# Kernel optimization log

Hardware: AMD Instinct MI355X
Metric: run time of the kernel (lower is better)

The kernel has to match this reference:

```python
import jax, jax.numpy as jnp
import numpy as np


def setup_inputs() -> dict:
    key = jax.random.key(0)
    k1, k2, k3, k4 = jax.random.split(key, 4)
    B, N, IN_DIM, QK_DIM = 8, 2048, 10, 32
    s = jax.random.normal(k1, (B, N, IN_DIM), dtype=jnp.float32)
    G = jax.random.uniform(k2, (B, N, N), dtype=jnp.float32)
    Wq = jax.random.normal(k3, (QK_DIM, IN_DIM), dtype=jnp.float32) * (1.0 / np.sqrt(IN_DIM))
    Wk = jax.random.normal(k4, (QK_DIM, IN_DIM), dtype=jnp.float32) * (1.0 / np.sqrt(IN_DIM))
    return {"s": s, "G": G, "Wq": Wq, "Wk": Wk}


def reference(s, G, Wq, Wk):
    # q, k: [B, N, qk_dim]  (nn.Linear with no bias: x @ W^T)
    q = jnp.einsum("bnd,qd->bnq", s, Wq)
    k = jnp.einsum("bnd,qd->bnq", s, Wk)
    # logits: [B, N, N]
    logits = jnp.einsum("bnq,bmq->bnm", q, k)
    w = jnp.square(logits) * G
    w = w / (jnp.sum(w, axis=-1, keepdims=True) + 1e-06)
    return w
```

## Files before the change

kernel.cpp:

```cpp
#include <hip/hip_runtime.h>
#include <stdint.h>

#define BB 8
#define NN 2048
#define IND 10
#define QK 32

typedef float f32x4 __attribute__((ext_vector_type(4)));

__global__ __launch_bounds__(256) void qk_kernel(
    const float* __restrict__ s,
    const float* __restrict__ Wq, const float* __restrict__ Wk,
    float* __restrict__ q_ws, float* __restrict__ kt_ws) {
  int t = blockIdx.x * 256 + threadIdx.x;
  int b  = t >> 16;
  int n  = (t >> 5) & (NN - 1);
  int qd = t & 31;
  const float* srow = s + (size_t)(b * NN + n) * IND;
  float acq = 0.f, ack = 0.f;
#pragma unroll
  for (int d = 0; d < IND; ++d) {
    float sv = srow[d];
    acq = fmaf(sv, Wq[qd * IND + d], acq);
    ack = fmaf(sv, Wk[qd * IND + d], ack);
  }
  q_ws[(size_t)(b * NN + n) * QK + qd] = acq;
  int w  = n >> 9;
  int m  = n & 511;
  int i  = (m & 255) >> 2;
  int jc = ((m < 256) ? 0 : 4) + (m & 3);
  int ev = qd >> 2, c = qd & 3;
  kt_ws[(((size_t)(b * 4 + w) * 4096) + (ev * 8 + jc) * 64 + i) * 4 + c] = ack;
}

__global__ __launch_bounds__(256, 2) void attn_kernel(
    const float* __restrict__ G,
    const float* __restrict__ q_ws, const float* __restrict__ kt_ws,
    float* __restrict__ out) {
  const int tid = threadIdx.x;
  const int b = blockIdx.y;
  const int r0 = blockIdx.x * 8;
  const int w = tid >> 6, lane = tid & 63;

  __shared__ float q_lds[4][256];
  __shared__ float red[4][8];

  {
    const float* qb = q_ws + ((size_t)b * NN + r0) * QK;
    *(float4*)&q_lds[w][4 * lane] = *(const float4*)&qb[4 * lane];
  }

  float acc[8][8];
#pragma unroll
  for (int r = 0; r < 8; ++r)
#pragma unroll
    for (int j = 0; j < 8; ++j) acc[r][j] = 0.f;

  const float4* kt =
      (const float4*)kt_ws + (size_t)(b * 4 + w) * 4096 + lane;

  float4 ka[8], kb[8];
#pragma unroll
  for (int j = 0; j < 8; ++j) ka[j] = kt[j * 64];

#pragma unroll
  for (int ev = 0; ev < 8; ++ev) {
    if (ev < 7) {
#pragma unroll
      for (int j = 0; j < 8; ++j) kb[j] = kt[((ev + 1) * 8 + j) * 64];
    }
#pragma unroll
    for (int r = 0; r < 8; ++r) {
      float q4[4];
      *(float4*)q4 = *(const float4*)&q_lds[w][r * 32 + ev * 4];
#pragma unroll
      for (int j = 0; j < 8; ++j) {
        acc[r][j] = fmaf(q4[0], ka[j].x, acc[r][j]);
        acc[r][j] = fmaf(q4[1], ka[j].y, acc[r][j]);
        acc[r][j] = fmaf(q4[2], ka[j].z, acc[r][j]);
        acc[r][j] = fmaf(q4[3], ka[j].w, acc[r][j]);
      }
    }
#pragma unroll
    for (int j = 0; j < 8; ++j) ka[j] = kb[j];
  }

  const float* gb = G + ((size_t)b * NN + r0) * NN + 512 * w + 4 * lane;
  float4 g0[8], g1[8];
#pragma unroll
  for (int r = 0; r < 8; ++r) {
    g0[r] = *(const float4*)(gb + (size_t)r * NN);
    g1[r] = *(const float4*)(gb + (size_t)r * NN + 256);
  }
  __builtin_amdgcn_sched_barrier(0);

  float rsum[8];
#pragma unroll
  for (int r = 0; r < 8; ++r) {
    float gg[8];
    *(float4*)&gg[0] = g0[r];
    *(float4*)&gg[4] = g1[r];
    float sum = 0.f;
#pragma unroll
    for (int j = 0; j < 8; ++j) {
      float v = acc[r][j];
      v = v * v * gg[j];
      acc[r][j] = v;
      sum += v;
    }
#pragma unroll
    for (int off = 32; off >= 1; off >>= 1) sum += __shfl_xor(sum, off, 64);
    rsum[r] = sum;
  }

  if ((tid & 63) == 0) {
#pragma unroll
    for (int r = 0; r < 8; ++r) red[w][r] = rsum[r];
  }
  __syncthreads();

  float inv[8];
#pragma unroll
  for (int r = 0; r < 8; ++r) {
    float total = red[0][r] + red[1][r] + red[2][r] + red[3][r];
    inv[r] = 1.0f / (total + 1e-6f);
  }

  float* ob = out + ((size_t)b * NN + r0) * NN + 512 * w + 4 * lane;
#pragma unroll
  for (int r = 0; r < 8; ++r) {
    f32x4 o0, o1;
    o0.x = acc[r][0] * inv[r]; o0.y = acc[r][1] * inv[r];
    o0.z = acc[r][2] * inv[r]; o0.w = acc[r][3] * inv[r];
    o1.x = acc[r][4] * inv[r]; o1.y = acc[r][5] * inv[r];
    o1.z = acc[r][6] * inv[r]; o1.w = acc[r][7] * inv[r];
    __builtin_nontemporal_store(o0, (f32x4*)(ob + (size_t)r * NN));
    __builtin_nontemporal_store(o1, (f32x4*)(ob + (size_t)r * NN + 256));
  }
}

extern "C" void kernel_launch(void* const* d_in, const int* in_sizes, int n_in,
                              void* d_out, int out_size, void* d_ws, size_t ws_size,
                              hipStream_t stream) {
  const float* s  = (const float*)d_in[0];
  const float* G  = (const float*)d_in[1];
  const float* Wq = (const float*)d_in[2];
  const float* Wk = (const float*)d_in[3];
  float* out = (float*)d_out;

  float* q_ws  = (float*)d_ws;
  float* kt_ws = q_ws + (size_t)BB * NN * QK;

  qk_kernel<<<(BB * NN * QK) / 256, 256, 0, stream>>>(s, Wq, Wk, q_ws, kt_ws);

  dim3 grid(NN / 8, BB);
  attn_kernel<<<grid, 256, 0, stream>>>(G, q_ws, kt_ws, out);
}
```

Baseline: 62.47 us.

## Prefetch G tile via direct global-to-LDS loads overlapping final QK step

Issues the G tile loads before the last q·k accumulation step. Five rows per wave go straight into LDS via global_load_lds and three rows go into registers, so the long-latency G fetch overlaps the remaining FMAs. A vmcnt(0) wait and scheduling barriers then gate the softmax-style normalization. The intent is to hide G memory latency without blowing up register pressure, at the cost of about 40KB of extra LDS per block, which may reduce occupancy.

```diff
diff --git a/kernel.cpp b/kernel.cpp
--- a/kernel.cpp
+++ b/kernel.cpp
@@ -33,6 +33,15 @@
   kt_ws[(((size_t)(b * 4 + w) * 4096) + (ev * 8 + jc) * 64 + i) * 4 + c] = ack;
 }
 
+__device__ __forceinline__ void gload_lds16(const float* src, float* lds_dst) {
+  __builtin_amdgcn_global_load_lds(
+      reinterpret_cast<const __attribute__((address_space(1))) uint32_t*>(
+          reinterpret_cast<uintptr_t>(src)),
+      reinterpret_cast<__attribute__((address_space(3))) uint32_t*>(
+          reinterpret_cast<uintptr_t>(lds_dst)),
+      16, 0, 0);
+}
+
 __global__ __launch_bounds__(256, 2) void attn_kernel(
     const float* __restrict__ G,
     const float* __restrict__ q_ws, const float* __restrict__ kt_ws,
@@ -42,6 +51,7 @@
   const int r0 = blockIdx.x * 8;
   const int w = tid >> 6, lane = tid & 63;
 
+  __shared__ float g_lds[4][5][512];
   __shared__ float q_lds[4][256];
   __shared__ float red[4][8];
 
@@ -64,11 +74,9 @@
   for (int j = 0; j < 8; ++j) ka[j] = kt[j * 64];
 
 #pragma unroll
-  for (int ev = 0; ev < 8; ++ev) {
-    if (ev < 7) {
+  for (int ev = 0; ev < 7; ++ev) {
 #pragma unroll
-      for (int j = 0; j < 8; ++j) kb[j] = kt[((ev + 1) * 8 + j) * 64];
-    }
+    for (int j = 0; j < 8; ++j) kb[j] = kt[((ev + 1) * 8 + j) * 64];
 #pragma unroll
     for (int r = 0; r < 8; ++r) {
       float q4[4];
@@ -85,21 +93,49 @@
     for (int j = 0; j < 8; ++j) ka[j] = kb[j];
   }
 
+  __builtin_amdgcn_sched_barrier(0);
+
   const float* gb = G + ((size_t)b * NN + r0) * NN + 512 * w + 4 * lane;
-  float4 g0[8], g1[8];
+#pragma unroll
+  for (int r = 0; r < 5; ++r) {
+    gload_lds16(gb + (size_t)r * NN, &g_lds[w][r][0]);
+    gload_lds16(gb + (size_t)r * NN + 256, &g_lds[w][r][256]);
+  }
+  f32x4 g5[3][2];
+#pragma unroll
+  for (int r = 0; r < 3; ++r) {
+    g5[r][0] = *(const f32x4*)(gb + (size_t)(5 + r) * NN);
+    g5[r][1] = *(const f32x4*)(gb + (size_t)(5 + r) * NN + 256);
+  }
+  __builtin_amdgcn_sched_barrier(0);
+
 #pragma unroll
   for (int r = 0; r < 8; ++r) {
-    g0[r] = *(const float4*)(gb + (size_t)r * NN);
-    g1[r] = *(const float4*)(gb + (size_t)r * NN + 256);
+    float q4[4];
+    *(float4*)q4 = *(const float4*)&q_lds[w][r * 32 + 28];
+#pragma unroll
+    for (int j = 0; j < 8; ++j) {
+      acc[r][j] = fmaf(q4[0], ka[j].x, acc[r][j]);
+      acc[r][j] = fmaf(q4[1], ka[j].y, acc[r][j]);
+      acc[r][j] = fmaf(q4[2], ka[j].z, acc[r][j]);
+      acc[r][j] = fmaf(q4[3], ka[j].w, acc[r][j]);
+    }
   }
+
+  asm volatile("s_waitcnt vmcnt(0)" ::: "memory");
   __builtin_amdgcn_sched_barrier(0);
 
   float rsum[8];
 #pragma unroll
   for (int r = 0; r < 8; ++r) {
     float gg[8];
-    *(float4*)&gg[0] = g0[r];
-    *(float4*)&gg[4] = g1[r];
+    if (r < 5) {
+      *(float4*)&gg[0] = *(const float4*)&g_lds[w][r][4 * lane];
+      *(float4*)&gg[4] = *(const float4*)&g_lds[w][r][256 + 4 * lane];
+    } else {
+      *(f32x4*)&gg[0] = g5[r - 5][0];
+      *(f32x4*)&gg[4] = g5[r - 5][1];
+    }
     float sum = 0.f;
 #pragma unroll
     for (int j = 0; j < 8; ++j) {
```

Result: slower. 70.59 us (+13.0%).
